# Kernel tuning notes

Hardware: AMD Instinct MI355X
Metric: run time of the kernel (lower is better)

## Reference

```python
import jax, jax.numpy as jnp
import numpy as np

TNEI = 2
TOPK = 4
NEIGH = 2 * TNEI + 1  # window size = 5


def _normalize(x, eps=1e-12):
    # matches torch F.normalize(dim=-1)
    n = jnp.linalg.norm(x, axis=-1, keepdims=True)
    return x / jnp.maximum(n, eps)


def setup_inputs() -> dict:
    key = jax.random.key(0)
    ks = jax.random.split(key, 10)
    B, T, C = 32, 256, 128
    x = jax.random.normal(ks[0], (B, T, C), jnp.float32)
    radj = jax.random.randint(ks[1], (B, T, T), 0, 2).astype(jnp.int32)
    inxs = jax.random.randint(ks[2], (B, T, TOPK), 0, T)
    s = 1.0 / np.sqrt(C)
    W_pf = jax.random.normal(ks[3], (C, C), jnp.float32) * s
    W_ns = jax.random.normal(ks[4], (C, C), jnp.float32) * s
    W_v = jax.random.normal(ks[5], (C, C), jnp.float32) * s
    v_pf = jax.random.normal(ks[6], (NEIGH,), jnp.float32)
    g_pf = jnp.linalg.norm(v_pf)[None]  # weight_norm gain, shape (1,)
    v_ns = jax.random.normal(ks[7], (TOPK,), jnp.float32)
    g_ns = jnp.linalg.norm(v_ns)[None]
    return dict(x=x, radj=radj, inxs=inxs, W_pf=W_pf, W_ns=W_ns, W_v=W_v,
                v_pf=v_pf, g_pf=g_pf, v_ns=v_ns, g_ns=g_ns)


def reference(x, radj, inxs, W_pf, W_ns, W_v, v_pf, g_pf, v_ns, g_ns):
    B, T, C = x.shape
    pf = _normalize(x @ W_pf.T)
    ns = _normalize(x @ W_ns.T)
    v = x @ W_v.T
    # windowed neighbor indices, identical to _tneigh_mask(mode='all')
    i = jnp.arange(T)
    start = jnp.clip(i - TNEI, 0, T - NEIGH)
    nbr = start[:, None] + jnp.arange(NEIGH)[None, :]  # (T, NEIGH)
    ctx = pf[:, nbr]  # (B, T, NEIGH, C) — replaces one-hot ctxinx einsum
    # pairwise window similarity: (B,T,T,n,n)
    sim = jnp.einsum('bxic,byjc->bxyij', ctx, ctx)
    # AdaptiveMaxPool2d((n,1)) == max over the last (key-window) axis
    sim_pf = sim.max(axis=-1)  # (B,T,T,n)
    w_pf = g_pf[0] * v_pf / jnp.linalg.norm(v_pf)  # weight-norm agg_pf
    sim_pf = jnp.einsum('bxyi,i->bxy', sim_pf, w_pf)
    # topk-neighbor branch: inxs gathers ns rows (replaces one-hot einsum)
    ns_q = ns[jnp.arange(B)[:, None, None], inxs]  # (B,T,TOPK,C)
    sim_ns = jnp.einsum('bxnc,byc->bxyn', ns_q, ns)  # (B,T,T,TOPK)
    w_ns = g_ns[0] * v_ns / jnp.linalg.norm(v_ns)  # weight-norm agg_ns
    sim_ns = jnp.einsum('bxyn,n->bxy', sim_ns, w_ns)
    # adjacency mask: 0 -> -1e22, >0 -> 0
    mask = jnp.where(radj == 0, jnp.float32(-1e22), jnp.float32(0.0))
    attn = jax.nn.softmax(sim_pf + sim_ns + mask, axis=-1)  # (B,T,T)
    return jnp.einsum('bkt,btd->bkd', attn, v)  # (B,T,C)
```

## Files before the change

### kernel.cpp

```cpp
#include <hip/hip_runtime.h>
#include <math.h>


#define TT 256
#define CC 128

using bf16x8 = __attribute__((ext_vector_type(8))) short;
using f32x4  = __attribute__((ext_vector_type(4))) float;

__device__ __forceinline__ short bf_hi(float x) {
    unsigned u = __float_as_uint(x);
    return (short)((u + 0x7FFFu + ((u >> 16) & 1u)) >> 16);
}
__device__ __forceinline__ void bf_split(float x, short& h, short& l) {
    h = bf_hi(x);
    float hf = __uint_as_float(((unsigned)(unsigned short)h) << 16);
    l = bf_hi(x - hf);
}
__device__ __forceinline__ float max5(float a, float b, float c, float d, float e) {
    return fmaxf(fmaxf(fmaxf(a, b), fmaxf(c, d)), e);
}

__global__ __launch_bounds__(256, 4) void proj_kernel(
    const float* __restrict__ x,
    const float* __restrict__ W0, const float* __restrict__ W1, const float* __restrict__ W2,
    float* __restrict__ pf, float* __restrict__ ns,
    short* __restrict__ vt_h, short* __restrict__ vt_l)
{
    __shared__ short Ah[32 * 40], Al[32 * 40];
    __shared__ short Bh[128 * 40], Bl[128 * 40];
    __shared__ float ssb[32][4];
    const int tid = threadIdx.x;
    const int row0 = blockIdx.x * 32;
    const int m = blockIdx.y;
    const float* __restrict__ W = (m == 0) ? W0 : (m == 1) ? W1 : W2;
    const int lane = tid & 63, wn = tid >> 6;
    const int quad = lane >> 4, lr = lane & 15;
    f32x4 z4 = {0.f, 0.f, 0.f, 0.f};
    f32x4 acc[2][2] = {{z4, z4}, {z4, z4}};

    for (int k0 = 0; k0 < CC; k0 += 32) {
        __syncthreads();
        {
            int r = tid >> 3, q = (tid & 7) * 4;
            float4 a4 = *(const float4*)&x[(row0 + r) * CC + k0 + q];
            short4 h4, l4;
            bf_split(a4.x, h4.x, l4.x); bf_split(a4.y, h4.y, l4.y);
            bf_split(a4.z, h4.z, l4.z); bf_split(a4.w, h4.w, l4.w);
            *(short4*)&Ah[r * 40 + q] = h4; *(short4*)&Al[r * 40 + q] = l4;
        }
        for (int i = 0; i < 4; i++) {
            int flat = i * 256 + tid, r = flat >> 3, q = (flat & 7) * 4;
            float4 b4 = *(const float4*)&W[r * CC + k0 + q];
            short4 h4, l4;
            bf_split(b4.x, h4.x, l4.x); bf_split(b4.y, h4.y, l4.y);
            bf_split(b4.z, h4.z, l4.z); bf_split(b4.w, h4.w, l4.w);
            *(short4*)&Bh[r * 40 + q] = h4; *(short4*)&Bl[r * 40 + q] = l4;
        }
        __syncthreads();
        bf16x8 ah[2], al[2], bh[2], bl[2];
        for (int ra = 0; ra < 2; ra++) {
            int ar = (16 * ra + lr) * 40 + quad * 8;
            ah[ra] = *(bf16x8*)&Ah[ar];
            al[ra] = *(bf16x8*)&Al[ar];
        }
        for (int tn = 0; tn < 2; tn++) {
            int br = (32 * wn + 16 * tn + lr) * 40 + quad * 8;
            bh[tn] = *(bf16x8*)&Bh[br];
            bl[tn] = *(bf16x8*)&Bl[br];
        }
        for (int ra = 0; ra < 2; ra++)
            for (int tn = 0; tn < 2; tn++) {
                acc[ra][tn] = __builtin_amdgcn_mfma_f32_16x16x32_bf16(ah[ra], bh[tn], acc[ra][tn], 0, 0, 0);
                acc[ra][tn] = __builtin_amdgcn_mfma_f32_16x16x32_bf16(ah[ra], bl[tn], acc[ra][tn], 0, 0, 0);
                acc[ra][tn] = __builtin_amdgcn_mfma_f32_16x16x32_bf16(al[ra], bh[tn], acc[ra][tn], 0, 0, 0);
            }
    }
    if (m < 2) {
        float* __restrict__ o = (m == 0) ? pf : ns;
        float ssp[2][4];
        for (int ra = 0; ra < 2; ra++)
            for (int reg = 0; reg < 4; reg++) {
                float s = acc[ra][0][reg] * acc[ra][0][reg]
                        + acc[ra][1][reg] * acc[ra][1][reg];
                for (int off = 1; off < 16; off <<= 1) s += __shfl_xor(s, off);
                ssp[ra][reg] = s;
            }
        if (lr == 0)
            for (int ra = 0; ra < 2; ra++)
                for (int reg = 0; reg < 4; reg++)
                    ssb[16 * ra + quad * 4 + reg][wn] = ssp[ra][reg];
        __syncthreads();
        for (int ra = 0; ra < 2; ra++)
            for (int reg = 0; reg < 4; reg++) {
                int ml = 16 * ra + quad * 4 + reg;
                float ss = ssb[ml][0] + ssb[ml][1] + ssb[ml][2] + ssb[ml][3];
                float inv = 1.f / fmaxf(sqrtf(ss), 1e-12f);
                int row = row0 + ml;
                for (int tn = 0; tn < 2; tn++)
                    o[row * CC + 32 * wn + 16 * tn + lr] = acc[ra][tn][reg] * inv;
            }
    } else {
        for (int ra = 0; ra < 2; ra++) {
            int rowbase = row0 + 16 * ra + quad * 4;
            int b = rowbase >> 8, t0 = rowbase & 255;
            for (int tn = 0; tn < 2; tn++) {
                int c = 32 * wn + 16 * tn + lr;
                short4 h4, l4;
                for (int reg = 0; reg < 4; reg++)
                    bf_split(acc[ra][tn][reg], ((short*)&h4)[reg], ((short*)&l4)[reg]);
                size_t o = ((size_t)b * CC + c) * TT + t0;
                *(short4*)&vt_h[o] = h4;
                *(short4*)&vt_l[o] = l4;
            }
        }
    }
}

__global__ __launch_bounds__(256, 4) void gram_mfma(
    const float* __restrict__ pf, const float* __restrict__ ns,
    const int* __restrict__ inxs, const float* __restrict__ v_ns,
    const float* __restrict__ g_ns, float* __restrict__ G, float* __restrict__ S)
{
    __shared__ short Ah[64 * 40], Al[64 * 40], Bh[64 * 40], Bl[64 * 40];
    const int tid = threadIdx.x;
    const int m0 = blockIdx.x * 64, n0 = blockIdx.y * 64;
    const int b = blockIdx.z >> 1, half = blockIdx.z & 1;
    const float* __restrict__ Pb = pf + (size_t)b * TT * CC;
    const float* __restrict__ Nb = ns + (size_t)b * TT * CC;
    const float* __restrict__ Bsrc = half ? Nb : Pb;

    float w0 = 0.f, w1 = 0.f, w2 = 0.f, w3 = 0.f;
    int4 id0 = {0, 0, 0, 0}, id1 = {0, 0, 0, 0};
    if (half) {
        float n2 = v_ns[0]*v_ns[0] + v_ns[1]*v_ns[1] + v_ns[2]*v_ns[2] + v_ns[3]*v_ns[3];
        float sc = g_ns[0] / sqrtf(n2);
        w0 = sc*v_ns[0]; w1 = sc*v_ns[1]; w2 = sc*v_ns[2]; w3 = sc*v_ns[3];
        id0 = *(const int4*)&inxs[(b * TT + m0 + (tid >> 3)) * 4];
        id1 = *(const int4*)&inxs[(b * TT + m0 + 32 + (tid >> 3)) * 4];
    }

    const int lane = tid & 63, wave = tid >> 6;
    const int wm = wave >> 1, wn = wave & 1;
    const int quad = lane >> 4, lr = lane & 15;
    f32x4 z4 = {0.f, 0.f, 0.f, 0.f};
    f32x4 acc[2][2] = {{z4, z4}, {z4, z4}};

    for (int k0 = 0; k0 < CC; k0 += 32) {
        __syncthreads();
        for (int i = 0; i < 2; i++) {
            int flat = i * 256 + tid, r = flat >> 3, q = (flat & 7) * 4;
            float4 a4;
            if (!half) {
                a4 = *(const float4*)&Pb[(m0 + r) * CC + k0 + q];
            } else {
                int4 id = i ? id1 : id0;
                float4 aa = *(const float4*)&Nb[id.x * CC + k0 + q];
                float4 ab = *(const float4*)&Nb[id.y * CC + k0 + q];
                float4 ac = *(const float4*)&Nb[id.z * CC + k0 + q];
                float4 ad = *(const float4*)&Nb[id.w * CC + k0 + q];
                a4.x = w0*aa.x + w1*ab.x + w2*ac.x + w3*ad.x;
                a4.y = w0*aa.y + w1*ab.y + w2*ac.y + w3*ad.y;
                a4.z = w0*aa.z + w1*ab.z + w2*ac.z + w3*ad.z;
                a4.w = w0*aa.w + w1*ab.w + w2*ac.w + w3*ad.w;
            }
            float4 b4 = *(const float4*)&Bsrc[(n0 + r) * CC + k0 + q];
            short4 h4, l4;
            bf_split(a4.x, h4.x, l4.x); bf_split(a4.y, h4.y, l4.y);
            bf_split(a4.z, h4.z, l4.z); bf_split(a4.w, h4.w, l4.w);
            *(short4*)&Ah[r * 40 + q] = h4; *(short4*)&Al[r * 40 + q] = l4;
            bf_split(b4.x, h4.x, l4.x); bf_split(b4.y, h4.y, l4.y);
            bf_split(b4.z, h4.z, l4.z); bf_split(b4.w, h4.w, l4.w);
            *(short4*)&Bh[r * 40 + q] = h4; *(short4*)&Bl[r * 40 + q] = l4;
        }
        __syncthreads();
        bf16x8 bh[2], bl[2];
        for (int tn = 0; tn < 2; tn++) {
            int br = (32 * wn + 16 * tn + lr) * 40 + quad * 8;
            bh[tn] = *(bf16x8*)&Bh[br];
            bl[tn] = *(bf16x8*)&Bl[br];
        }
        for (int tm = 0; tm < 2; tm++) {
            int ar = (32 * wm + 16 * tm + lr) * 40 + quad * 8;
            bf16x8 ah = *(bf16x8*)&Ah[ar];
            bf16x8 al = *(bf16x8*)&Al[ar];
            for (int tn = 0; tn < 2; tn++) {
                acc[tm][tn] = __builtin_amdgcn_mfma_f32_16x16x32_bf16(ah, bh[tn], acc[tm][tn], 0, 0, 0);
                acc[tm][tn] = __builtin_amdgcn_mfma_f32_16x16x32_bf16(ah, bl[tn], acc[tm][tn], 0, 0, 0);
                acc[tm][tn] = __builtin_amdgcn_mfma_f32_16x16x32_bf16(al, bh[tn], acc[tm][tn], 0, 0, 0);
            }
        }
    }
    float* __restrict__ Cb = (half ? S : G) + (size_t)b * TT * TT;
    for (int tm = 0; tm < 2; tm++)
        for (int tn = 0; tn < 2; tn++) {
            int rb = m0 + 32 * wm + 16 * tm + quad * 4;
            int cb = n0 + 32 * wn + 16 * tn + lr;
            for (int reg = 0; reg < 4; reg++)
                Cb[(size_t)(rb + reg) * TT + cb] = acc[tm][tn][reg];
        }
}

__global__ __launch_bounds__(256, 2) void fused_smax_pv(
    const float* __restrict__ G, const float* __restrict__ S,
    const int* __restrict__ radj, const float* __restrict__ v_pf,
    const float* __restrict__ g_pf,
    const short* __restrict__ vt_h, const short* __restrict__ vt_l,
    float* __restrict__ out)
{
    __shared__ float Gs[20 * 256];
    __shared__ float RM[20 * 256];
    __shared__ short ATH[16 * 264];
    __shared__ short ATL[16 * 264];
    __shared__ float RD[64];
    __shared__ float RMX[64];
    const int tid = threadIdx.x;
    const int xt = blockIdx.x, b = blockIdx.y;
    const int x0 = xt * 16;
    const int rbase = min(max(x0 - 2, 0), TT - 5);
    for (int i = 0; i < 5; i++) {
        int flat = i * 256 + tid, ri = flat >> 6, q = (flat & 63) * 4;
        int r = min(rbase + ri, TT - 1);
        *(float4*)&Gs[ri * 256 + q] = *(const float4*)&G[(size_t)b * TT * TT + r * TT + q];
    }
    float n2 = 0.f;
    for (int i = 0; i < 5; i++) n2 += v_pf[i] * v_pf[i];
    float sc = g_pf[0] / sqrtf(n2);
    float wpf[5];
    for (int i = 0; i < 5; i++) wpf[i] = sc * v_pf[i];
    __syncthreads();
    for (int t = 0; t < 5; t++) {
        int task = t * 256 + tid;
        int i = task >> 6, g = task & 63;
        const float* row = &Gs[i * 256];
        float4 X = *(float4*)&row[4 * g];
        float m0_, m1_, m2_, m3_;
        if (g == 0) {
            float4 N = *(float4*)&row[4];
            float mx = fmaxf(fmaxf(X.x, X.y), fmaxf(X.z, X.w));
            m0_ = m1_ = m2_ = fmaxf(mx, N.x);
            m3_ = max5(X.y, X.z, X.w, N.x, N.y);
        } else if (g == 63) {
            float4 P = *(float4*)&row[248];
            m0_ = max5(P.z, P.w, X.x, X.y, X.z);
            float mx = fmaxf(fmaxf(X.x, X.y), fmaxf(X.z, X.w));
            m1_ = m2_ = m3_ = fmaxf(P.w, mx);
        } else {
            float4 P = *(float4*)&row[4 * g - 4];
            float4 N = *(float4*)&row[4 * g + 4];
            m0_ = max5(P.z, P.w, X.x, X.y, X.z);
            m1_ = max5(P.w, X.x, X.y, X.z, X.w);
            m2_ = max5(X.x, X.y, X.z, X.w, N.x);
            m3_ = max5(X.y, X.z, X.w, N.x, N.y);
        }
        float4 o4 = {m0_, m1_, m2_, m3_};
        *(float4*)&RM[i * 256 + 4 * g] = o4;
    }
    __syncthreads();
    const int y = tid;
    const size_t sb = (size_t)b * TT * TT;
    float lv[16];
    if (xt > 0 && xt < 15) {
        float rm[20];
        #pragma unroll
        for (int r = 0; r < 20; r++) rm[r] = RM[r * 256 + y];
        #pragma unroll
        for (int xi = 0; xi < 16; xi++) {
            float s = wpf[0] * rm[xi];
            #pragma unroll
            for (int i = 1; i < 5; i++) s = fmaf(wpf[i], rm[xi + i], s);
            lv[xi] = s;
        }
    } else {
        for (int xi = 0; xi < 16; xi++) {
            int sxr = min(max(x0 + xi - 2, 0), TT - 5) - rbase;
            float s = 0.f;
            for (int i = 0; i < 5; i++) s = fmaf(wpf[i], RM[(sxr + i) * 256 + y], s);
            lv[xi] = s;
        }
    }
    for (int xi = 0; xi < 16; xi++) {
        lv[xi] += S[sb + (x0 + xi) * TT + y];
        if (radj[sb + (x0 + xi) * TT + y] == 0) lv[xi] += -1e22f;
    }
    const int lane = tid & 63, wv = tid >> 6;
    for (int xi = 0; xi < 16; xi++) {
        float v = lv[xi];
        for (int o = 32; o; o >>= 1) v = fmaxf(v, __shfl_xor(v, o));
        if (lane == 0) RMX[xi * 4 + wv] = v;
    }
    __syncthreads();
    for (int xi = 0; xi < 16; xi++) {
        float mx = fmaxf(fmaxf(RMX[xi * 4], RMX[xi * 4 + 1]),
                         fmaxf(RMX[xi * 4 + 2], RMX[xi * 4 + 3]));
        float e = __expf(lv[xi] - mx);
        short h, l;
        bf_split(e, h, l);
        ATH[xi * 264 + y] = h;
        ATL[xi * 264 + y] = l;
        for (int o = 32; o; o >>= 1) e += __shfl_xor(e, o);
        if (lane == 0) RD[xi * 4 + wv] = e;
    }
    __syncthreads();
    const int quad = lane >> 4, lr = lane & 15;
    const int c0 = wv * 32;
    const short* __restrict__ vhb = vt_h + (size_t)b * CC * TT;
    const short* __restrict__ vlb = vt_l + (size_t)b * CC * TT;
    const int ar0 = (c0 + lr) * TT, ar1 = ar0 + 16 * TT;
    f32x4 z4 = {0.f, 0.f, 0.f, 0.f};
    f32x4 acc[2] = {z4, z4};
    #pragma unroll
    for (int k0 = 0; k0 < TT; k0 += 32) {
        int ko = k0 + quad * 8;
        bf16x8 bh = *(bf16x8*)&ATH[lr * 264 + ko];
        bf16x8 bl = *(bf16x8*)&ATL[lr * 264 + ko];
        bf16x8 a0h = *(const bf16x8*)&vhb[ar0 + ko];
        bf16x8 a0l = *(const bf16x8*)&vlb[ar0 + ko];
        bf16x8 a1h = *(const bf16x8*)&vhb[ar1 + ko];
        bf16x8 a1l = *(const bf16x8*)&vlb[ar1 + ko];
        acc[0] = __builtin_amdgcn_mfma_f32_16x16x32_bf16(a0h, bh, acc[0], 0, 0, 0);
        acc[0] = __builtin_amdgcn_mfma_f32_16x16x32_bf16(a0h, bl, acc[0], 0, 0, 0);
        acc[0] = __builtin_amdgcn_mfma_f32_16x16x32_bf16(a0l, bh, acc[0], 0, 0, 0);
        acc[1] = __builtin_amdgcn_mfma_f32_16x16x32_bf16(a1h, bh, acc[1], 0, 0, 0);
        acc[1] = __builtin_amdgcn_mfma_f32_16x16x32_bf16(a1h, bl, acc[1], 0, 0, 0);
        acc[1] = __builtin_amdgcn_mfma_f32_16x16x32_bf16(a1l, bh, acc[1], 0, 0, 0);
    }
    float sm = RD[lr * 4] + RD[lr * 4 + 1] + RD[lr * 4 + 2] + RD[lr * 4 + 3];
    float rinv = 1.f / sm;
    for (int tm = 0; tm < 2; tm++) {
        float4 r;
        r.x = acc[tm][0] * rinv; r.y = acc[tm][1] * rinv;
        r.z = acc[tm][2] * rinv; r.w = acc[tm][3] * rinv;
        *(float4*)&out[(size_t)b * TT * CC + (x0 + lr) * CC + c0 + 16 * tm + quad * 4] = r;
    }
}

extern "C" void kernel_launch(void* const* d_in, const int* in_sizes, int n_in,
                              void* d_out, int out_size, void* d_ws, size_t ws_size,
                              hipStream_t stream) {
    const float* x    = (const float*)d_in[0];
    const int*   radj = (const int*)d_in[1];
    const int*   inxs = (const int*)d_in[2];
    const float* Wpf  = (const float*)d_in[3];
    const float* Wns  = (const float*)d_in[4];
    const float* Wv   = (const float*)d_in[5];
    const float* v_pf = (const float*)d_in[6];
    const float* g_pf = (const float*)d_in[7];
    const float* v_ns = (const float*)d_in[8];
    const float* g_ns = (const float*)d_in[9];
    float* out = (float*)d_out;

    char* base = (char*)d_ws;
    float* pf   = (float*)(base);
    float* ns   = (float*)(base + (4u << 20));
    short* vt_h = (short*)(base + (8u << 20));
    short* vt_l = (short*)(base + (10u << 20));
    float* G    = (float*)(base + (12u << 20));
    float* S    = (float*)(base + (20u << 20));

    proj_kernel<<<dim3(256, 3), 256, 0, stream>>>(x, Wpf, Wns, Wv, pf, ns, vt_h, vt_l);
    gram_mfma<<<dim3(4, 4, 64), 256, 0, stream>>>(pf, ns, inxs, v_ns, g_ns, G, S);
    fused_smax_pv<<<dim3(16, 32), 256, 0, stream>>>(G, S, radj, v_pf, g_pf,
                                                    vt_h, vt_l, out);
}
```

Before: 126.6 us.

## Fuse three kernels into one cooperative persistent kernel with grid syncs

Replaces the projection, Gram and softmax-PV launches with a single cooperative kernel of 512 blocks. Each block loops over the work units of each phase, with grid.sync between phases, and the phases share LDS through a union. This removes launch gaps and inter-kernel overhead. In exchange it fixes the grid size, drops occupancy to 2 blocks per CU, and adds grid-wide barrier costs.

```diff
diff --git a/kernel.cpp b/kernel.cpp
--- a/kernel.cpp
+++ b/kernel.cpp
@@ -1,5 +1,8 @@
 #include <hip/hip_runtime.h>
+#include <hip/hip_cooperative_groups.h>
 #include <math.h>
+
+namespace cg = cooperative_groups;
 
 
 #define TT 256
@@ -21,317 +24,325 @@
     return fmaxf(fmaxf(fmaxf(a, b), fmaxf(c, d)), e);
 }
 
-__global__ __launch_bounds__(256, 4) void proj_kernel(
-    const float* __restrict__ x,
-    const float* __restrict__ W0, const float* __restrict__ W1, const float* __restrict__ W2,
+struct LdsA {
+    short Ah[32 * 40], Al[32 * 40];
+    short Bh[128 * 40], Bl[128 * 40];
+    float ssb[32][4];
+};
+struct LdsB {
+    short Ah[64 * 40], Al[64 * 40], Bh[64 * 40], Bl[64 * 40];
+};
+struct LdsC {
+    float Gs[20 * 256];
+    float RM[20 * 256];
+    short ATH[16 * 264], ATL[16 * 264];
+    float RD[64], RMX[64];
+};
+union LdsU { LdsA a; LdsB b; LdsC c; };
+
+__global__ __launch_bounds__(256, 2) void mega_kernel(
+    const float* __restrict__ x, const int* __restrict__ radj,
+    const int* __restrict__ inxs,
+    const float* __restrict__ Wpf, const float* __restrict__ Wns,
+    const float* __restrict__ Wv,
+    const float* __restrict__ v_pf, const float* __restrict__ g_pf,
+    const float* __restrict__ v_ns, const float* __restrict__ g_ns,
     float* __restrict__ pf, float* __restrict__ ns,
-    short* __restrict__ vt_h, short* __restrict__ vt_l)
-{
-    __shared__ short Ah[32 * 40], Al[32 * 40];
-    __shared__ short Bh[128 * 40], Bl[128 * 40];
-    __shared__ float ssb[32][4];
-    const int tid = threadIdx.x;
-    const int row0 = blockIdx.x * 32;
-    const int m = blockIdx.y;
-    const float* __restrict__ W = (m == 0) ? W0 : (m == 1) ? W1 : W2;
-    const int lane = tid & 63, wn = tid >> 6;
-    const int quad = lane >> 4, lr = lane & 15;
-    f32x4 z4 = {0.f, 0.f, 0.f, 0.f};
-    f32x4 acc[2][2] = {{z4, z4}, {z4, z4}};
-
-    for (int k0 = 0; k0 < CC; k0 += 32) {
-        __syncthreads();
-        {
-            int r = tid >> 3, q = (tid & 7) * 4;
-            float4 a4 = *(const float4*)&x[(row0 + r) * CC + k0 + q];
-            short4 h4, l4;
-            bf_split(a4.x, h4.x, l4.x); bf_split(a4.y, h4.y, l4.y);
-            bf_split(a4.z, h4.z, l4.z); bf_split(a4.w, h4.w, l4.w);
-            *(short4*)&Ah[r * 40 + q] = h4; *(short4*)&Al[r * 40 + q] = l4;
-        }
-        for (int i = 0; i < 4; i++) {
-            int flat = i * 256 + tid, r = flat >> 3, q = (flat & 7) * 4;
-            float4 b4 = *(const float4*)&W[r * CC + k0 + q];
-            short4 h4, l4;
-            bf_split(b4.x, h4.x, l4.x); bf_split(b4.y, h4.y, l4.y);
-            bf_split(b4.z, h4.z, l4.z); bf_split(b4.w, h4.w, l4.w);
-            *(short4*)&Bh[r * 40 + q] = h4; *(short4*)&Bl[r * 40 + q] = l4;
-        }
-        __syncthreads();
-        bf16x8 ah[2], al[2], bh[2], bl[2];
-        for (int ra = 0; ra < 2; ra++) {
-            int ar = (16 * ra + lr) * 40 + quad * 8;
-            ah[ra] = *(bf16x8*)&Ah[ar];
-            al[ra] = *(bf16x8*)&Al[ar];
-        }
-        for (int tn = 0; tn < 2; tn++) {
-            int br = (32 * wn + 16 * tn + lr) * 40 + quad * 8;
-            bh[tn] = *(bf16x8*)&Bh[br];
-            bl[tn] = *(bf16x8*)&Bl[br];
-        }
-        for (int ra = 0; ra < 2; ra++)
-            for (int tn = 0; tn < 2; tn++) {
-                acc[ra][tn] = __builtin_amdgcn_mfma_f32_16x16x32_bf16(ah[ra], bh[tn], acc[ra][tn], 0, 0, 0);
-                acc[ra][tn] = __builtin_amdgcn_mfma_f32_16x16x32_bf16(ah[ra], bl[tn], acc[ra][tn], 0, 0, 0);
-                acc[ra][tn] = __builtin_amdgcn_mfma_f32_16x16x32_bf16(al[ra], bh[tn], acc[ra][tn], 0, 0, 0);
-            }
-    }
-    if (m < 2) {
-        float* __restrict__ o = (m == 0) ? pf : ns;
-        float ssp[2][4];
-        for (int ra = 0; ra < 2; ra++)
-            for (int reg = 0; reg < 4; reg++) {
-                float s = acc[ra][0][reg] * acc[ra][0][reg]
-                        + acc[ra][1][reg] * acc[ra][1][reg];
-                for (int off = 1; off < 16; off <<= 1) s += __shfl_xor(s, off);
-                ssp[ra][reg] = s;
-            }
-        if (lr == 0)
-            for (int ra = 0; ra < 2; ra++)
-                for (int reg = 0; reg < 4; reg++)
-                    ssb[16 * ra + quad * 4 + reg][wn] = ssp[ra][reg];
-        __syncthreads();
-        for (int ra = 0; ra < 2; ra++)
-            for (int reg = 0; reg < 4; reg++) {
-                int ml = 16 * ra + quad * 4 + reg;
-                float ss = ssb[ml][0] + ssb[ml][1] + ssb[ml][2] + ssb[ml][3];
-                float inv = 1.f / fmaxf(sqrtf(ss), 1e-12f);
-                int row = row0 + ml;
-                for (int tn = 0; tn < 2; tn++)
-                    o[row * CC + 32 * wn + 16 * tn + lr] = acc[ra][tn][reg] * inv;
-            }
-    } else {
-        for (int ra = 0; ra < 2; ra++) {
-            int rowbase = row0 + 16 * ra + quad * 4;
-            int b = rowbase >> 8, t0 = rowbase & 255;
-            for (int tn = 0; tn < 2; tn++) {
-                int c = 32 * wn + 16 * tn + lr;
-                short4 h4, l4;
-                for (int reg = 0; reg < 4; reg++)
-                    bf_split(acc[ra][tn][reg], ((short*)&h4)[reg], ((short*)&l4)[reg]);
-                size_t o = ((size_t)b * CC + c) * TT + t0;
-                *(short4*)&vt_h[o] = h4;
-                *(short4*)&vt_l[o] = l4;
-            }
-        }
-    }
-}
-
-__global__ __launch_bounds__(256, 4) void gram_mfma(
-    const float* __restrict__ pf, const float* __restrict__ ns,
-    const int* __restrict__ inxs, const float* __restrict__ v_ns,
-    const float* __restrict__ g_ns, float* __restrict__ G, float* __restrict__ S)
-{
-    __shared__ short Ah[64 * 40], Al[64 * 40], Bh[64 * 40], Bl[64 * 40];
-    const int tid = threadIdx.x;
-    const int m0 = blockIdx.x * 64, n0 = blockIdx.y * 64;
-    const int b = blockIdx.z >> 1, half = blockIdx.z & 1;
-    const float* __restrict__ Pb = pf + (size_t)b * TT * CC;
-    const float* __restrict__ Nb = ns + (size_t)b * TT * CC;
-    const float* __restrict__ Bsrc = half ? Nb : Pb;
-
-    float w0 = 0.f, w1 = 0.f, w2 = 0.f, w3 = 0.f;
-    int4 id0 = {0, 0, 0, 0}, id1 = {0, 0, 0, 0};
-    if (half) {
-        float n2 = v_ns[0]*v_ns[0] + v_ns[1]*v_ns[1] + v_ns[2]*v_ns[2] + v_ns[3]*v_ns[3];
-        float sc = g_ns[0] / sqrtf(n2);
-        w0 = sc*v_ns[0]; w1 = sc*v_ns[1]; w2 = sc*v_ns[2]; w3 = sc*v_ns[3];
-        id0 = *(const int4*)&inxs[(b * TT + m0 + (tid >> 3)) * 4];
-        id1 = *(const int4*)&inxs[(b * TT + m0 + 32 + (tid >> 3)) * 4];
-    }
-
-    const int lane = tid & 63, wave = tid >> 6;
-    const int wm = wave >> 1, wn = wave & 1;
-    const int quad = lane >> 4, lr = lane & 15;
-    f32x4 z4 = {0.f, 0.f, 0.f, 0.f};
-    f32x4 acc[2][2] = {{z4, z4}, {z4, z4}};
-
-    for (int k0 = 0; k0 < CC; k0 += 32) {
-        __syncthreads();
-        for (int i = 0; i < 2; i++) {
-            int flat = i * 256 + tid, r = flat >> 3, q = (flat & 7) * 4;
-            float4 a4;
-            if (!half) {
-                a4 = *(const float4*)&Pb[(m0 + r) * CC + k0 + q];
-            } else {
-                int4 id = i ? id1 : id0;
-                float4 aa = *(const float4*)&Nb[id.x * CC + k0 + q];
-                float4 ab = *(const float4*)&Nb[id.y * CC + k0 + q];
-                float4 ac = *(const float4*)&Nb[id.z * CC + k0 + q];
-                float4 ad = *(const float4*)&Nb[id.w * CC + k0 + q];
-                a4.x = w0*aa.x + w1*ab.x + w2*ac.x + w3*ad.x;
-                a4.y = w0*aa.y + w1*ab.y + w2*ac.y + w3*ad.y;
-                a4.z = w0*aa.z + w1*ab.z + w2*ac.z + w3*ad.z;
-                a4.w = w0*aa.w + w1*ab.w + w2*ac.w + w3*ad.w;
-            }
-            float4 b4 = *(const float4*)&Bsrc[(n0 + r) * CC + k0 + q];
-            short4 h4, l4;
-            bf_split(a4.x, h4.x, l4.x); bf_split(a4.y, h4.y, l4.y);
-            bf_split(a4.z, h4.z, l4.z); bf_split(a4.w, h4.w, l4.w);
-            *(short4*)&Ah[r * 40 + q] = h4; *(short4*)&Al[r * 40 + q] = l4;
-            bf_split(b4.x, h4.x, l4.x); bf_split(b4.y, h4.y, l4.y);
-            bf_split(b4.z, h4.z, l4.z); bf_split(b4.w, h4.w, l4.w);
-            *(short4*)&Bh[r * 40 + q] = h4; *(short4*)&Bl[r * 40 + q] = l4;
-        }
-        __syncthreads();
-        bf16x8 bh[2], bl[2];
-        for (int tn = 0; tn < 2; tn++) {
-            int br = (32 * wn + 16 * tn + lr) * 40 + quad * 8;
-            bh[tn] = *(bf16x8*)&Bh[br];
-            bl[tn] = *(bf16x8*)&Bl[br];
-        }
-        for (int tm = 0; tm < 2; tm++) {
-            int ar = (32 * wm + 16 * tm + lr) * 40 + quad * 8;
-            bf16x8 ah = *(bf16x8*)&Ah[ar];
-            bf16x8 al = *(bf16x8*)&Al[ar];
-            for (int tn = 0; tn < 2; tn++) {
-                acc[tm][tn] = __builtin_amdgcn_mfma_f32_16x16x32_bf16(ah, bh[tn], acc[tm][tn], 0, 0, 0);
-                acc[tm][tn] = __builtin_amdgcn_mfma_f32_16x16x32_bf16(ah, bl[tn], acc[tm][tn], 0, 0, 0);
-                acc[tm][tn] = __builtin_amdgcn_mfma_f32_16x16x32_bf16(al, bh[tn], acc[tm][tn], 0, 0, 0);
-            }
-        }
-    }
-    float* __restrict__ Cb = (half ? S : G) + (size_t)b * TT * TT;
-    for (int tm = 0; tm < 2; tm++)
-        for (int tn = 0; tn < 2; tn++) {
-            int rb = m0 + 32 * wm + 16 * tm + quad * 4;
-            int cb = n0 + 32 * wn + 16 * tn + lr;
-            for (int reg = 0; reg < 4; reg++)
-                Cb[(size_t)(rb + reg) * TT + cb] = acc[tm][tn][reg];
-        }
-}
-
-__global__ __launch_bounds__(256, 2) void fused_smax_pv(
-    const float* __restrict__ G, const float* __restrict__ S,
-    const int* __restrict__ radj, const float* __restrict__ v_pf,
-    const float* __restrict__ g_pf,
-    const short* __restrict__ vt_h, const short* __restrict__ vt_l,
+    short* __restrict__ vt_h, short* __restrict__ vt_l,
+    float* __restrict__ G, float* __restrict__ S,
     float* __restrict__ out)
 {
-    __shared__ float Gs[20 * 256];
-    __shared__ float RM[20 * 256];
-    __shared__ short ATH[16 * 264];
-    __shared__ short ATL[16 * 264];
-    __shared__ float RD[64];
-    __shared__ float RMX[64];
-    const int tid = threadIdx.x;
-    const int xt = blockIdx.x, b = blockIdx.y;
-    const int x0 = xt * 16;
-    const int rbase = min(max(x0 - 2, 0), TT - 5);
-    for (int i = 0; i < 5; i++) {
-        int flat = i * 256 + tid, ri = flat >> 6, q = (flat & 63) * 4;
-        int r = min(rbase + ri, TT - 1);
-        *(float4*)&Gs[ri * 256 + q] = *(const float4*)&G[(size_t)b * TT * TT + r * TT + q];
+    cg::grid_group grid = cg::this_grid();
+    __shared__ LdsU u;
+    const int tid = threadIdx.x, bid = blockIdx.x;
+    const int lane = tid & 63;
+    const int quad = lane >> 4, lr = lane & 15;
+
+    for (int unit = bid; unit < 768; unit += 512) {
+        const int row0 = (unit & 255) * 32;
+        const int m = unit >> 8;
+        const float* __restrict__ W = (m == 0) ? Wpf : (m == 1) ? Wns : Wv;
+        const int wn = tid >> 6;
+        f32x4 z4 = {0.f, 0.f, 0.f, 0.f};
+        f32x4 acc[2][2] = {{z4, z4}, {z4, z4}};
+
+        for (int k0 = 0; k0 < CC; k0 += 32) {
+            __syncthreads();
+            {
+                int r = tid >> 3, q = (tid & 7) * 4;
+                float4 a4 = *(const float4*)&x[(row0 + r) * CC + k0 + q];
+                short4 h4, l4;
+                bf_split(a4.x, h4.x, l4.x); bf_split(a4.y, h4.y, l4.y);
+                bf_split(a4.z, h4.z, l4.z); bf_split(a4.w, h4.w, l4.w);
+                *(short4*)&u.a.Ah[r * 40 + q] = h4; *(short4*)&u.a.Al[r * 40 + q] = l4;
+            }
+            for (int i = 0; i < 4; i++) {
+                int flat = i * 256 + tid, r = flat >> 3, q = (flat & 7) * 4;
+                float4 b4 = *(const float4*)&W[r * CC + k0 + q];
+                short4 h4, l4;
+                bf_split(b4.x, h4.x, l4.x); bf_split(b4.y, h4.y, l4.y);
+                bf_split(b4.z, h4.z, l4.z); bf_split(b4.w, h4.w, l4.w);
+                *(short4*)&u.a.Bh[r * 40 + q] = h4; *(short4*)&u.a.Bl[r * 40 + q] = l4;
+            }
+            __syncthreads();
+            bf16x8 ah[2], al[2], bh[2], bl[2];
+            for (int ra = 0; ra < 2; ra++) {
+                int ar = (16 * ra + lr) * 40 + quad * 8;
+                ah[ra] = *(bf16x8*)&u.a.Ah[ar];
+                al[ra] = *(bf16x8*)&u.a.Al[ar];
+            }
+            for (int tn = 0; tn < 2; tn++) {
+                int br = (32 * wn + 16 * tn + lr) * 40 + quad * 8;
+                bh[tn] = *(bf16x8*)&u.a.Bh[br];
+                bl[tn] = *(bf16x8*)&u.a.Bl[br];
+            }
+            for (int ra = 0; ra < 2; ra++)
+                for (int tn = 0; tn < 2; tn++) {
+                    acc[ra][tn] = __builtin_amdgcn_mfma_f32_16x16x32_bf16(ah[ra], bh[tn], acc[ra][tn], 0, 0, 0);
+                    acc[ra][tn] = __builtin_amdgcn_mfma_f32_16x16x32_bf16(ah[ra], bl[tn], acc[ra][tn], 0, 0, 0);
+                    acc[ra][tn] = __builtin_amdgcn_mfma_f32_16x16x32_bf16(al[ra], bh[tn], acc[ra][tn], 0, 0, 0);
+                }
+        }
+        if (m < 2) {
+            float* __restrict__ o = (m == 0) ? pf : ns;
+            float ssp[2][4];
+            for (int ra = 0; ra < 2; ra++)
+                for (int reg = 0; reg < 4; reg++) {
+                    float s = acc[ra][0][reg] * acc[ra][0][reg]
+                            + acc[ra][1][reg] * acc[ra][1][reg];
+                    for (int off = 1; off < 16; off <<= 1) s += __shfl_xor(s, off);
+                    ssp[ra][reg] = s;
+                }
+            if (lr == 0)
+                for (int ra = 0; ra < 2; ra++)
+                    for (int reg = 0; reg < 4; reg++)
+                        u.a.ssb[16 * ra + quad * 4 + reg][wn] = ssp[ra][reg];
+            __syncthreads();
+            for (int ra = 0; ra < 2; ra++)
+                for (int reg = 0; reg < 4; reg++) {
+                    int ml = 16 * ra + quad * 4 + reg;
+                    float ss = u.a.ssb[ml][0] + u.a.ssb[ml][1] + u.a.ssb[ml][2] + u.a.ssb[ml][3];
+                    float inv = 1.f / fmaxf(sqrtf(ss), 1e-12f);
+                    int row = row0 + ml;
+                    for (int tn = 0; tn < 2; tn++)
+                        o[row * CC + 32 * wn + 16 * tn + lr] = acc[ra][tn][reg] * inv;
+                }
+        } else {
+            for (int ra = 0; ra < 2; ra++) {
+                int rowbase = row0 + 16 * ra + quad * 4;
+                int b = rowbase >> 8, t0 = rowbase & 255;
+                for (int tn = 0; tn < 2; tn++) {
+                    int c = 32 * wn + 16 * tn + lr;
+                    short4 h4, l4;
+                    for (int reg = 0; reg < 4; reg++)
+                        bf_split(acc[ra][tn][reg], ((short*)&h4)[reg], ((short*)&l4)[reg]);
+                    size_t o = ((size_t)b * CC + c) * TT + t0;
+                    *(short4*)&vt_h[o] = h4;
+                    *(short4*)&vt_l[o] = l4;
+                }
+            }
+        }
+        __syncthreads();
     }
-    float n2 = 0.f;
-    for (int i = 0; i < 5; i++) n2 += v_pf[i] * v_pf[i];
-    float sc = g_pf[0] / sqrtf(n2);
-    float wpf[5];
-    for (int i = 0; i < 5; i++) wpf[i] = sc * v_pf[i];
-    __syncthreads();
-    for (int t = 0; t < 5; t++) {
-        int task = t * 256 + tid;
-        int i = task >> 6, g = task & 63;
-        const float* row = &Gs[i * 256];
-        float4 X = *(float4*)&row[4 * g];
-        float m0_, m1_, m2_, m3_;
-        if (g == 0) {
-            float4 N = *(float4*)&row[4];
-            float mx = fmaxf(fmaxf(X.x, X.y), fmaxf(X.z, X.w));
-            m0_ = m1_ = m2_ = fmaxf(mx, N.x);
-            m3_ = max5(X.y, X.z, X.w, N.x, N.y);
-        } else if (g == 63) {
-            float4 P = *(float4*)&row[248];
-            m0_ = max5(P.z, P.w, X.x, X.y, X.z);
-            float mx = fmaxf(fmaxf(X.x, X.y), fmaxf(X.z, X.w));
-            m1_ = m2_ = m3_ = fmaxf(P.w, mx);
+    grid.sync();
+
+    for (int unitB = bid; unitB < 1024; unitB += 512) {
+        const int m0 = (unitB & 3) * 64, n0 = ((unitB >> 2) & 3) * 64;
+        const int bz = unitB >> 4;
+        const int b = bz >> 1, half = bz & 1;
+        const float* __restrict__ Pb = pf + (size_t)b * TT * CC;
+        const float* __restrict__ Nb = ns + (size_t)b * TT * CC;
+        const float* __restrict__ Bsrc = half ? Nb : Pb;
+
+        float w0 = 0.f, w1 = 0.f, w2 = 0.f, w3 = 0.f;
+        int4 id0 = {0, 0, 0, 0}, id1 = {0, 0, 0, 0};
+        if (half) {
+            float n2 = v_ns[0]*v_ns[0] + v_ns[1]*v_ns[1] + v_ns[2]*v_ns[2] + v_ns[3]*v_ns[3];
+            float sc = g_ns[0] / sqrtf(n2);
+            w0 = sc*v_ns[0]; w1 = sc*v_ns[1]; w2 = sc*v_ns[2]; w3 = sc*v_ns[3];
+            id0 = *(const int4*)&inxs[(b * TT + m0 + (tid >> 3)) * 4];
+            id1 = *(const int4*)&inxs[(b * TT + m0 + 32 + (tid >> 3)) * 4];
+        }
+        const int wave = tid >> 6;
+        const int wm = wave >> 1, wn = wave & 1;
+        f32x4 z4 = {0.f, 0.f, 0.f, 0.f};
+        f32x4 acc[2][2] = {{z4, z4}, {z4, z4}};
+
+        for (int k0 = 0; k0 < CC; k0 += 32) {
+            __syncthreads();
+            for (int i = 0; i < 2; i++) {
+                int flat = i * 256 + tid, r = flat >> 3, q = (flat & 7) * 4;
+                float4 a4;
+                if (!half) {
+                    a4 = *(const float4*)&Pb[(m0 + r) * CC + k0 + q];
+                } else {
+                    int4 id = i ? id1 : id0;
+                    float4 aa = *(const float4*)&Nb[id.x * CC + k0 + q];
+                    float4 ab = *(const float4*)&Nb[id.y * CC + k0 + q];
+                    float4 ac = *(const float4*)&Nb[id.z * CC + k0 + q];
+                    float4 ad = *(const float4*)&Nb[id.w * CC + k0 + q];
+                    a4.x = w0*aa.x + w1*ab.x + w2*ac.x + w3*ad.x;
+                    a4.y = w0*aa.y + w1*ab.y + w2*ac.y + w3*ad.y;
+                    a4.z = w0*aa.z + w1*ab.z + w2*ac.z + w3*ad.z;
+                    a4.w = w0*aa.w + w1*ab.w + w2*ac.w + w3*ad.w;
+                }
+                float4 b4 = *(const float4*)&Bsrc[(n0 + r) * CC + k0 + q];
+                short4 h4, l4;
+                bf_split(a4.x, h4.x, l4.x); bf_split(a4.y, h4.y, l4.y);
+                bf_split(a4.z, h4.z, l4.z); bf_split(a4.w, h4.w, l4.w);
+                *(short4*)&u.b.Ah[r * 40 + q] = h4; *(short4*)&u.b.Al[r * 40 + q] = l4;
+                bf_split(b4.x, h4.x, l4.x); bf_split(b4.y, h4.y, l4.y);
+                bf_split(b4.z, h4.z, l4.z); bf_split(b4.w, h4.w, l4.w);
+                *(short4*)&u.b.Bh[r * 40 + q] = h4; *(short4*)&u.b.Bl[r * 40 + q] = l4;
+            }
+            __syncthreads();
+            bf16x8 bh[2], bl[2];
+            for (int tn = 0; tn < 2; tn++) {
+                int br = (32 * wn + 16 * tn + lr) * 40 + quad * 8;
+                bh[tn] = *(bf16x8*)&u.b.Bh[br];
+                bl[tn] = *(bf16x8*)&u.b.Bl[br];
+            }
+            for (int tm = 0; tm < 2; tm++) {
+                int ar = (32 * wm + 16 * tm + lr) * 40 + quad * 8;
+                bf16x8 ah = *(bf16x8*)&u.b.Ah[ar];
+                bf16x8 al = *(bf16x8*)&u.b.Al[ar];
+                for (int tn = 0; tn < 2; tn++) {
+                    acc[tm][tn] = __builtin_amdgcn_mfma_f32_16x16x32_bf16(ah, bh[tn], acc[tm][tn], 0, 0, 0);
+                    acc[tm][tn] = __builtin_amdgcn_mfma_f32_16x16x32_bf16(ah, bl[tn], acc[tm][tn], 0, 0, 0);
+                    acc[tm][tn] = __builtin_amdgcn_mfma_f32_16x16x32_bf16(al, bh[tn], acc[tm][tn], 0, 0, 0);
+                }
+            }
+        }
+        float* __restrict__ Cb = (half ? S : G) + (size_t)b * TT * TT;
+        for (int tm = 0; tm < 2; tm++)
+            for (int tn = 0; tn < 2; tn++) {
+                int rb = m0 + 32 * wm + 16 * tm + quad * 4;
+                int cb = n0 + 32 * wn + 16 * tn + lr;
+                for (int reg = 0; reg < 4; reg++)
+                    Cb[(size_t)(rb + reg) * TT + cb] = acc[tm][tn][reg];
+            }
+        __syncthreads();
+    }
+    grid.sync();
+
+    {
+        const int xt = bid & 15, b = bid >> 4;
+        const int x0 = xt * 16;
+        const int rbase = min(max(x0 - 2, 0), TT - 5);
+        for (int i = 0; i < 5; i++) {
+            int flat = i * 256 + tid, ri = flat >> 6, q = (flat & 63) * 4;
+            int r = min(rbase + ri, TT - 1);
+            *(float4*)&u.c.Gs[ri * 256 + q] = *(const float4*)&G[(size_t)b * TT * TT + r * TT + q];
+        }
+        float n2 = 0.f;
+        for (int i = 0; i < 5; i++) n2 += v_pf[i] * v_pf[i];
+        float sc = g_pf[0] / sqrtf(n2);
+        float wpf[5];
+        for (int i = 0; i < 5; i++) wpf[i] = sc * v_pf[i];
+        __syncthreads();
+        for (int t = 0; t < 5; t++) {
+            int task = t * 256 + tid;
+            int i = task >> 6, g = task & 63;
+            const float* row = &u.c.Gs[i * 256];
+            float4 X = *(float4*)&row[4 * g];
+            float m0_, m1_, m2_, m3_;
+            if (g == 0) {
+                float4 N = *(float4*)&row[4];
+                float mx = fmaxf(fmaxf(X.x, X.y), fmaxf(X.z, X.w));
+                m0_ = m1_ = m2_ = fmaxf(mx, N.x);
+                m3_ = max5(X.y, X.z, X.w, N.x, N.y);
+            } else if (g == 63) {
+                float4 P = *(float4*)&row[248];
+                m0_ = max5(P.z, P.w, X.x, X.y, X.z);
+                float mx = fmaxf(fmaxf(X.x, X.y), fmaxf(X.z, X.w));
+                m1_ = m2_ = m3_ = fmaxf(P.w, mx);
+            } else {
+                float4 P = *(float4*)&row[4 * g - 4];
+                float4 N = *(float4*)&row[4 * g + 4];
+                m0_ = max5(P.z, P.w, X.x, X.y, X.z);
+                m1_ = max5(P.w, X.x, X.y, X.z, X.w);
+                m2_ = max5(X.x, X.y, X.z, X.w, N.x);
+                m3_ = max5(X.y, X.z, X.w, N.x, N.y);
+            }
+            float4 o4 = {m0_, m1_, m2_, m3_};
+            *(float4*)&u.c.RM[i * 256 + 4 * g] = o4;
+        }
+        __syncthreads();
+        const int y = tid;
+        const size_t sb = (size_t)b * TT * TT;
+        float lv[16];
+        if (xt > 0 && xt < 15) {
+            float rm[20];
+            #pragma unroll
+            for (int r = 0; r < 20; r++) rm[r] = u.c.RM[r * 256 + y];
+            #pragma unroll
+            for (int xi = 0; xi < 16; xi++) {
+                float s = wpf[0] * rm[xi];
+                #pragma unroll
+                for (int i = 1; i < 5; i++) s = fmaf(wpf[i], rm[xi + i], s);
+                lv[xi] = s;
+            }
         } else {
-            float4 P = *(float4*)&row[4 * g - 4];
-            float4 N = *(float4*)&row[4 * g + 4];
-            m0_ = max5(P.z, P.w, X.x, X.y, X.z);
-            m1_ = max5(P.w, X.x, X.y, X.z, X.w);
-            m2_ = max5(X.x, X.y, X.z, X.w, N.x);
-            m3_ = max5(X.y, X.z, X.w, N.x, N.y);
-        }
-        float4 o4 = {m0_, m1_, m2_, m3_};
-        *(float4*)&RM[i * 256 + 4 * g] = o4;
-    }
-    __syncthreads();
-    const int y = tid;
-    const size_t sb = (size_t)b * TT * TT;
-    float lv[16];
-    if (xt > 0 && xt < 15) {
-        float rm[20];
+            for (int xi = 0; xi < 16; xi++) {
+                int sxr = min(max(x0 + xi - 2, 0), TT - 5) - rbase;
+                float s = 0.f;
+                for (int i = 0; i < 5; i++) s = fmaf(wpf[i], u.c.RM[(sxr + i) * 256 + y], s);
+                lv[xi] = s;
+            }
+        }
+        for (int xi = 0; xi < 16; xi++) {
+            lv[xi] += S[sb + (x0 + xi) * TT + y];
+            if (radj[sb + (x0 + xi) * TT + y] == 0) lv[xi] += -1e22f;
+        }
+        const int wv = tid >> 6;
+        for (int xi = 0; xi < 16; xi++) {
+            float v = lv[xi];
+            for (int o = 32; o; o >>= 1) v = fmaxf(v, __shfl_xor(v, o));
+            if (lane == 0) u.c.RMX[xi * 4 + wv] = v;
+        }
+        __syncthreads();
+        for (int xi = 0; xi < 16; xi++) {
+            float mx = fmaxf(fmaxf(u.c.RMX[xi * 4], u.c.RMX[xi * 4 + 1]),
+                             fmaxf(u.c.RMX[xi * 4 + 2], u.c.RMX[xi * 4 + 3]));
+            float e = __expf(lv[xi] - mx);
+            short h, l;
+            bf_split(e, h, l);
+            u.c.ATH[xi * 264 + y] = h;
+            u.c.ATL[xi * 264 + y] = l;
+            for (int o = 32; o; o >>= 1) e += __shfl_xor(e, o);
+            if (lane == 0) u.c.RD[xi * 4 + wv] = e;
+        }
+        __syncthreads();
+        const int c0 = wv * 32;
+        const short* __restrict__ vhb = vt_h + (size_t)b * CC * TT;
+        const short* __restrict__ vlb = vt_l + (size_t)b * CC * TT;
+        const int ar0 = (c0 + lr) * TT, ar1 = ar0 + 16 * TT;
+        f32x4 z4 = {0.f, 0.f, 0.f, 0.f};
+        f32x4 acc[2] = {z4, z4};
         #pragma unroll
-        for (int r = 0; r < 20; r++) rm[r] = RM[r * 256 + y];
-        #pragma unroll
-        for (int xi = 0; xi < 16; xi++) {
-            float s = wpf[0] * rm[xi];
-            #pragma unroll
-            for (int i = 1; i < 5; i++) s = fmaf(wpf[i], rm[xi + i], s);
-            lv[xi] = s;
-        }
-    } else {
-        for (int xi = 0; xi < 16; xi++) {
-            int sxr = min(max(x0 + xi - 2, 0), TT - 5) - rbase;
-            float s = 0.f;
-            for (int i = 0; i < 5; i++) s = fmaf(wpf[i], RM[(sxr + i) * 256 + y], s);
-            lv[xi] = s;
-        }
-    }
-    for (int xi = 0; xi < 16; xi++) {
-        lv[xi] += S[sb + (x0 + xi) * TT + y];
-        if (radj[sb + (x0 + xi) * TT + y] == 0) lv[xi] += -1e22f;
-    }
-    const int lane = tid & 63, wv = tid >> 6;
-    for (int xi = 0; xi < 16; xi++) {
-        float v = lv[xi];
-        for (int o = 32; o; o >>= 1) v = fmaxf(v, __shfl_xor(v, o));
-        if (lane == 0) RMX[xi * 4 + wv] = v;
-    }
-    __syncthreads();
-    for (int xi = 0; xi < 16; xi++) {
-        float mx = fmaxf(fmaxf(RMX[xi * 4], RMX[xi * 4 + 1]),
-                         fmaxf(RMX[xi * 4 + 2], RMX[xi * 4 + 3]));
-        float e = __expf(lv[xi] - mx);
-        short h, l;
-        bf_split(e, h, l);
-        ATH[xi * 264 + y] = h;
-        ATL[xi * 264 + y] = l;
-        for (int o = 32; o; o >>= 1) e += __shfl_xor(e, o);
-        if (lane == 0) RD[xi * 4 + wv] = e;
-    }
-    __syncthreads();
-    const int quad = lane >> 4, lr = lane & 15;
-    const int c0 = wv * 32;
-    const short* __restrict__ vhb = vt_h + (size_t)b * CC * TT;
-    const short* __restrict__ vlb = vt_l + (size_t)b * CC * TT;
-    const int ar0 = (c0 + lr) * TT, ar1 = ar0 + 16 * TT;
-    f32x4 z4 = {0.f, 0.f, 0.f, 0.f};
-    f32x4 acc[2] = {z4, z4};
-    #pragma unroll
-    for (int k0 = 0; k0 < TT; k0 += 32) {
-        int ko = k0 + quad * 8;
-        bf16x8 bh = *(bf16x8*)&ATH[lr * 264 + ko];
-        bf16x8 bl = *(bf16x8*)&ATL[lr * 264 + ko];
-        bf16x8 a0h = *(const bf16x8*)&vhb[ar0 + ko];
-        bf16x8 a0l = *(const bf16x8*)&vlb[ar0 + ko];
-        bf16x8 a1h = *(const bf16x8*)&vhb[ar1 + ko];
-        bf16x8 a1l = *(const bf16x8*)&vlb[ar1 + ko];
-        acc[0] = __builtin_amdgcn_mfma_f32_16x16x32_bf16(a0h, bh, acc[0], 0, 0, 0);
-        acc[0] = __builtin_amdgcn_mfma_f32_16x16x32_bf16(a0h, bl, acc[0], 0, 0, 0);
-        acc[0] = __builtin_amdgcn_mfma_f32_16x16x32_bf16(a0l, bh, acc[0], 0, 0, 0);
-        acc[1] = __builtin_amdgcn_mfma_f32_16x16x32_bf16(a1h, bh, acc[1], 0, 0, 0);
-        acc[1] = __builtin_amdgcn_mfma_f32_16x16x32_bf16(a1h, bl, acc[1], 0, 0, 0);
-        acc[1] = __builtin_amdgcn_mfma_f32_16x16x32_bf16(a1l, bh, acc[1], 0, 0, 0);
-    }
-    float sm = RD[lr * 4] + RD[lr * 4 + 1] + RD[lr * 4 + 2] + RD[lr * 4 + 3];
-    float rinv = 1.f / sm;
-    for (int tm = 0; tm < 2; tm++) {
-        float4 r;
-        r.x = acc[tm][0] * rinv; r.y = acc[tm][1] * rinv;
-        r.z = acc[tm][2] * rinv; r.w = acc[tm][3] * rinv;
-        *(float4*)&out[(size_t)b * TT * CC + (x0 + lr) * CC + c0 + 16 * tm + quad * 4] = r;
+        for (int k0 = 0; k0 < TT; k0 += 32) {
+            int ko = k0 + quad * 8;
+            bf16x8 bh = *(bf16x8*)&u.c.ATH[lr * 264 + ko];
+            bf16x8 bl = *(bf16x8*)&u.c.ATL[lr * 264 + ko];
+            bf16x8 a0h = *(const bf16x8*)&vhb[ar0 + ko];
+            bf16x8 a0l = *(const bf16x8*)&vlb[ar0 + ko];
+            bf16x8 a1h = *(const bf16x8*)&vhb[ar1 + ko];
+            bf16x8 a1l = *(const bf16x8*)&vlb[ar1 + ko];
+            acc[0] = __builtin_amdgcn_mfma_f32_16x16x32_bf16(a0h, bh, acc[0], 0, 0, 0);
+            acc[0] = __builtin_amdgcn_mfma_f32_16x16x32_bf16(a0h, bl, acc[0], 0, 0, 0);
+            acc[0] = __builtin_amdgcn_mfma_f32_16x16x32_bf16(a0l, bh, acc[0], 0, 0, 0);
+            acc[1] = __builtin_amdgcn_mfma_f32_16x16x32_bf16(a1h, bh, acc[1], 0, 0, 0);
+            acc[1] = __builtin_amdgcn_mfma_f32_16x16x32_bf16(a1h, bl, acc[1], 0, 0, 0);
+            acc[1] = __builtin_amdgcn_mfma_f32_16x16x32_bf16(a1l, bh, acc[1], 0, 0, 0);
+        }
+        float sm = u.c.RD[lr * 4] + u.c.RD[lr * 4 + 1] + u.c.RD[lr * 4 + 2] + u.c.RD[lr * 4 + 3];
+        float rinv = 1.f / sm;
+        for (int tm = 0; tm < 2; tm++) {
+            float4 r;
+            r.x = acc[tm][0] * rinv; r.y = acc[tm][1] * rinv;
+            r.z = acc[tm][2] * rinv; r.w = acc[tm][3] * rinv;
+            *(float4*)&out[(size_t)b * TT * CC + (x0 + lr) * CC + c0 + 16 * tm + quad * 4] = r;
+        }
     }
 }
 
@@ -358,8 +369,13 @@
     float* G    = (float*)(base + (12u << 20));
     float* S    = (float*)(base + (20u << 20));
 
-    proj_kernel<<<dim3(256, 3), 256, 0, stream>>>(x, Wpf, Wns, Wv, pf, ns, vt_h, vt_l);
-    gram_mfma<<<dim3(4, 4, 64), 256, 0, stream>>>(pf, ns, inxs, v_ns, g_ns, G, S);
-    fused_smax_pv<<<dim3(16, 32), 256, 0, stream>>>(G, S, radj, v_pf, g_pf,
-                                                    vt_h, vt_l, out);
-}
+    void* args[] = {
+        (void*)&x, (void*)&radj, (void*)&inxs,
+        (void*)&Wpf, (void*)&Wns, (void*)&Wv,
+        (void*)&v_pf, (void*)&g_pf, (void*)&v_ns, (void*)&g_ns,
+        (void*)&pf, (void*)&ns, (void*)&vt_h, (void*)&vt_l,
+        (void*)&G, (void*)&S, (void*)&out
+    };
+    hipLaunchCooperativeKernel((const void*)mega_kernel, dim3(512), dim3(256),
+                               args, 0, stream);
+}
```

Result: slower. 263.7 us (+108.2%).
